# Kernel optimization log

Measured on AMD Instinct MI355X. Metric: run time of the kernel, lower is better.

Reference implementation:

```python
import jax, jax.numpy as jnp
import numpy as np

# ---- static config (matches init_kwargs) ----
C, H, W = 3, 224, 224
P = 16
KH, KW = H // P, W // P          # 14, 14
N_PATCH = KH * KW                # 196
PATCH_ELEMS = C * P * P          # 768
D = 768
HEADS = 12
Y = 64                            # head dim
M = 3072                          # hopfield memories
N_MASK = 100
NSTEPS = 12
ALPHA = 0.1
BETA = 1.0 / float(np.sqrt(Y))
EPS = 1e-5
B = 16


def lnorm(x, gamma, delta):
    # EnergyLayerNorm: scalar gamma, vector delta, RMS of centered x
    xm = x - x.mean(-1, keepdims=True)
    return gamma * xm / jnp.sqrt((xm * xm).mean(-1, keepdims=True) + EPS) + delta


def energy(g, Wq, Wk, Xi):
    # attention energy: -(1/beta) sum_h sum_q logsumexp_k(beta * q_h . k_h)
    q = jnp.einsum('nd,hdy->nhy', g, Wq)
    k = jnp.einsum('nd,hdy->nhy', g, Wk)
    A = jnp.einsum('nhy,mhy->hnm', q, k)                    # [H, N, N]
    e_att = -(1.0 / BETA) * jax.nn.logsumexp(BETA * A, axis=-1).sum()
    # hopfield energy: -0.5 * sum relu(g @ Xi)^2
    hid = jax.nn.relu(g @ Xi)                                # [N, M]
    e_hn = -0.5 * jnp.sum(hid * hid)
    return e_att + e_hn


def patchify(img):
    # (C, H, W) -> (n_patches, C*P*P), matching '... c (kh h) (kw w) -> ... (kh kw) c h w' then flatten c h w
    x = img.reshape(C, KH, P, KW, P).transpose(1, 3, 0, 2, 4)
    return x.reshape(N_PATCH, PATCH_ELEMS)


def unpatchify(p):
    # (n_patches, C, P, P) -> (C, H, W)
    return p.reshape(KH, KW, C, P, P).transpose(2, 0, 3, 1, 4).reshape(C, H, W)


def forward_single(img, mask, enc_W, enc_b, dec_W, dec_b, cls_token, mask_token,
                   pos_embed, Wq, Wk, Xi, gamma, delta):
    tok = patchify(img) @ enc_W + enc_b                      # [N_PATCH, D]
    (idx,) = jnp.nonzero(mask == 1, size=N_MASK, fill_value=0)
    tok = tok.at[idx].set(mask_token)                        # corrupt masked tokens
    x = jnp.concatenate([cls_token[None], tok], axis=0) + pos_embed  # [N_PATCH+1, D]
    grad_e = jax.grad(energy)
    for _ in range(NSTEPS):
        g = lnorm(x, gamma, delta)
        x = x - ALPHA * grad_e(g, Wq, Wk, Xi)
    x = x[1:]
    g = lnorm(x, gamma, delta)
    dec = (g @ dec_W + dec_b).reshape(N_PATCH, C, P, P)
    return unpatchify(dec)


def setup_inputs() -> dict:
    key = jax.random.key(0)
    ks = jax.random.split(key, 10)
    return {
        'x': jax.random.normal(ks[0], (B, C, H, W), dtype=jnp.float32),
        'mask': jax.random.randint(ks[1], (B, N_PATCH), 0, 2, dtype=jnp.int32),
        'enc_W': 0.1 * jax.random.normal(ks[2], (PATCH_ELEMS, D), dtype=jnp.float32),
        'enc_b': jnp.zeros((D,), dtype=jnp.float32),
        'dec_W': 0.1 * jax.random.normal(ks[3], (D, PATCH_ELEMS), dtype=jnp.float32),
        'dec_b': jnp.zeros((PATCH_ELEMS,), dtype=jnp.float32),
        'cls_token': 0.002 * jax.random.normal(ks[4], (D,), dtype=jnp.float32),
        'mask_token': 0.002 * jax.random.normal(ks[5], (D,), dtype=jnp.float32),
        'pos_embed': 0.002 * jax.random.normal(ks[6], (1 + N_PATCH, D), dtype=jnp.float32),
        'Wq': 0.02 * jax.random.normal(ks[7], (HEADS, D, Y), dtype=jnp.float32),
        'Wk': 0.02 * jax.random.normal(ks[8], (HEADS, D, Y), dtype=jnp.float32),
        'Xi': 0.02 * jax.random.normal(ks[9], (D, M), dtype=jnp.float32),
        'gamma': jnp.ones((), dtype=jnp.float32),
        'delta': jnp.zeros((D,), dtype=jnp.float32),
    }


def reference(x, mask, enc_W, enc_b, dec_W, dec_b, cls_token, mask_token,
              pos_embed, Wq, Wk, Xi, gamma, delta):
    f = jax.vmap(forward_single, in_axes=(0, 0) + (None,) * 12)
    return f(x, mask, enc_W, enc_b, dec_W, dec_b, cls_token, mask_token,
             pos_embed, Wq, Wk, Xi, gamma, delta)
```

## Files before the change

kernel.cpp:

```cpp
#include <hip/hip_runtime.h>
#include <math.h>

#define C_      3
#define H_      224
#define W_      224
#define KH_     14
#define KW_     14
#define NPATCH  196
#define PELEMS  768
#define D_      768
#define HEADS_  12
#define Y_      64
#define MHID    3072
#define NMASK   100
#define NSTEPS  12
#define ALPHA_  0.1f
#define BETA_   0.125f
#define EPS_    1e-5f
#define B_      16
#define NTOK    197
#define ROWS    (B_*NTOK)
#define MPAD    3200
#define QKLD    1536
#define PACKLD  4608
#define W2LD    4608
#define KSPLIT  4

typedef short short8 __attribute__((ext_vector_type(8)));
typedef unsigned short ushort8 __attribute__((ext_vector_type(8)));
typedef float floatx4 __attribute__((ext_vector_type(4)));

__device__ __forceinline__ unsigned short f2bf(float f) {
    union { float f; unsigned u; } v; v.f = f;
    unsigned r = (v.u + 0x7FFFu + ((v.u >> 16) & 1u)) >> 16;
    return (unsigned short)r;
}
__device__ __forceinline__ float bf2f(unsigned short u) {
    union { unsigned u; float f; } v; v.u = ((unsigned)u) << 16;
    return v.f;
}

__device__ __forceinline__ void async_cp16(const void* g, void* l) {
    __builtin_amdgcn_global_load_lds(
        (const __attribute__((address_space(1))) unsigned int*)g,
        (__attribute__((address_space(3))) unsigned int*)l, 16, 0, 0);
}

template<int OUT_MODE, bool RELU, bool HAS_BIAS>
__global__ __launch_bounds__(256) void mfma_gemm(
    const unsigned short* __restrict__ A, int lda,
    const unsigned short* __restrict__ B, int ldb,
    void* __restrict__ Cout, int ldc, void* __restrict__ Cout2,
    const float* __restrict__ bias, int K)
{
    __shared__ alignas(16) unsigned short ldsA[2][64 * 32];
    __shared__ alignas(16) unsigned short ldsB[2][128 * 32];

    const int bx = blockIdx.x, by = blockIdx.y;
    const int koff = (OUT_MODE == 4) ? blockIdx.z * K : 0;

    const int t    = threadIdx.x;
    const int wave = t >> 6;
    const int lane = t & 63;
    const int row0 = by << 6;
    const int col0 = bx << 7;
    const int wm = (wave & 1) << 5;
    const int wn = (wave >> 1) << 6;
    const int r  = lane & 15;
    const int qd = lane >> 4;

    const unsigned short* Abase = A + (size_t)row0 * lda + koff;
    const unsigned short* Bbase = B + (size_t)col0 * ldb + koff;

    floatx4 acc[2][4];
#pragma unroll
    for (int i = 0; i < 2; ++i)
#pragma unroll
        for (int j = 0; j < 4; ++j)
            acc[i][j] = (floatx4){0.f, 0.f, 0.f, 0.f};

    const int crow = t >> 2;
    const int coff = (t & 3) << 3;
    for (int k0 = 0; k0 < K; k0 += 64) {
#pragma unroll
        for (int kb = 0; kb < 2; ++kb) {
            const int kk = k0 + kb * 32;
            async_cp16(Abase + (size_t)crow * lda + kk + coff,
                       ldsA[kb] + (wave << 9));
            async_cp16(Bbase + (size_t)crow * ldb + kk + coff,
                       ldsB[kb] + (wave << 9));
            async_cp16(Bbase + (size_t)(64 + crow) * ldb + kk + coff,
                       ldsB[kb] + 2048 + (wave << 9));
        }
        __syncthreads();
#pragma unroll
        for (int kb = 0; kb < 2; ++kb) {
            short8 af[2], bfr[4];
#pragma unroll
            for (int i = 0; i < 2; ++i)
                af[i]  = *(const short8*)&ldsA[kb][(wm + (i << 4) + r) * 32 + (qd << 3)];
#pragma unroll
            for (int j = 0; j < 4; ++j)
                bfr[j] = *(const short8*)&ldsB[kb][(wn + (j << 4) + r) * 32 + (qd << 3)];
#pragma unroll
            for (int i = 0; i < 2; ++i)
#pragma unroll
                for (int j = 0; j < 4; ++j)
                    acc[i][j] = __builtin_amdgcn_mfma_f32_16x16x32_bf16(
                                    af[i], bfr[j], acc[i][j], 0, 0, 0);
        }
        __syncthreads();
    }

#pragma unroll
    for (int i = 0; i < 2; ++i) {
#pragma unroll
        for (int j = 0; j < 4; ++j) {
            int cc = col0 + wn + (j << 4) + r;
#pragma unroll
            for (int reg = 0; reg < 4; ++reg) {
                int rr = row0 + wm + (i << 4) + (qd << 2) + reg;
                float v = acc[i][j][reg];
                if (HAS_BIAS) v += bias[cc];
                if (RELU)     v = fmaxf(v, 0.f);
                if (OUT_MODE == 1)
                    ((unsigned short*)Cout)[(size_t)rr * ldc + cc] = f2bf(v);
                else if (OUT_MODE == 3) {
                    if (cc < QKLD)
                        ((unsigned short*)Cout)[(size_t)rr * QKLD + cc] = f2bf(v);
                    else
                        ((unsigned short*)Cout2)[(size_t)rr * PACKLD + (cc - QKLD)]
                            = f2bf(fmaxf(v, 0.f));
                } else if (OUT_MODE == 4)
                    atomicAdd(&((float*)Cout)[(size_t)rr * ldc + cc], ALPHA_ * v);
                else
                    ((float*)Cout)[(size_t)rr * ldc + cc] = v;
            }
        }
    }
}

__global__ __launch_bounds__(512) void attn_fused_kernel(
    const unsigned short* __restrict__ qk,
    unsigned short* __restrict__ pack)
{
    __shared__ alignas(16) unsigned short Ks[208 * 72];
    __shared__ alignas(16) unsigned short Kt[64 * 232];
    __shared__ alignas(16) unsigned short Qc[32 * 72];
    __shared__ alignas(16) unsigned short Qtc[64 * 40];
    __shared__ alignas(16) unsigned short Pb[32 * 232];
    __shared__ alignas(16) unsigned short PTb[208 * 40];
    __shared__ alignas(16) float Pm[32 * 212];

    const int bh = blockIdx.x;
    const int h = bh % HEADS_, b = bh / HEADS_;
    const int t = threadIdx.x;
    const int lane = t & 63, wave = t >> 6;
    const int ln15 = lane & 15, quad = lane >> 4;
    const size_t rowbase = (size_t)(b * NTOK) * QKLD;
    const int hoff = h * 64;

    for (int idx = t; idx < 208 * 8; idx += 512) {
        int m = idx >> 3, c8 = idx & 7;
        uint4 v = (uint4){0, 0, 0, 0};
        if (m < NTOK)
            v = *(const uint4*)&qk[rowbase + (size_t)m * QKLD + 768 + hoff + c8 * 8];
        *(uint4*)&Ks[m * 72 + c8 * 8] = v;
    }
    for (int idx = t; idx < (32 * 232) / 8; idx += 512)
        *(uint4*)&Pb[idx * 8] = (uint4){0, 0, 0, 0};
    for (int idx = t; idx < (208 * 40) / 8; idx += 512)
        *(uint4*)&PTb[idx * 8] = (uint4){0, 0, 0, 0};
    __syncthreads();

    for (int idx = t; idx < 64 * 112; idx += 512) {
        int y = idx / 112, mp = idx % 112;
        int m0 = 2 * mp;
        unsigned lo = (m0     < 208) ? Ks[(m0    ) * 72 + y] : 0u;
        unsigned hi = (m0 + 1 < 208) ? Ks[(m0 + 1) * 72 + y] : 0u;
        *(unsigned*)&Kt[y * 232 + m0] = lo | (hi << 16);
    }
    __syncthreads();

    floatx4 gk[7];
#pragma unroll
    for (int i = 0; i < 7; ++i) gk[i] = (floatx4){0.f, 0.f, 0.f, 0.f};

    for (int nc = 0; nc < 7; ++nc) {
        const int n0 = nc * 32;
        const int csz = (NTOK - n0 < 32) ? (NTOK - n0) : 32;

        for (int idx = t; idx < 32 * 8; idx += 512) {
            int nn = idx >> 3, c8 = idx & 7;
            uint4 v = (uint4){0, 0, 0, 0};
            if (nn < csz)
                v = *(const uint4*)&qk[rowbase + (size_t)(n0 + nn) * QKLD + hoff + c8 * 8];
            *(uint4*)&Qc[nn * 72 + c8 * 8] = v;
        }
        __syncthreads();

        for (int idx = t; idx < 64 * 16; idx += 512) {
            int y = idx >> 4, np = idx & 15;
            unsigned lo = Qc[(2 * np    ) * 72 + y];
            unsigned hi = Qc[(2 * np + 1) * 72 + y];
            *(unsigned*)&Qtc[y * 40 + 2 * np] = lo | (hi << 16);
        }

        {
            short8 aq[2][2];
#pragma unroll
            for (int nt = 0; nt < 2; ++nt)
#pragma unroll
                for (int kb = 0; kb < 2; ++kb)
                    aq[nt][kb] = *(const short8*)
                        &Qc[(nt * 16 + ln15) * 72 + kb * 32 + quad * 8];

            for (int mt = wave; mt < 13; mt += 8) {
                short8 b0 = *(const short8*)&Ks[(mt * 16 + ln15) * 72 + quad * 8];
                short8 b1 = *(const short8*)&Ks[(mt * 16 + ln15) * 72 + 32 + quad * 8];
                floatx4 s0 = (floatx4){0.f, 0.f, 0.f, 0.f};
                floatx4 s1 = (floatx4){0.f, 0.f, 0.f, 0.f};
                s0 = __builtin_amdgcn_mfma_f32_16x16x32_bf16(aq[0][0], b0, s0, 0, 0, 0);
                s0 = __builtin_amdgcn_mfma_f32_16x16x32_bf16(aq[0][1], b1, s0, 0, 0, 0);
                s1 = __builtin_amdgcn_mfma_f32_16x16x32_bf16(aq[1][0], b0, s1, 0, 0, 0);
                s1 = __builtin_amdgcn_mfma_f32_16x16x32_bf16(aq[1][1], b1, s1, 0, 0, 0);
#pragma unroll
                for (int reg = 0; reg < 4; ++reg) {
                    Pm[(quad * 4 + reg) * 212 + mt * 16 + ln15]      = s0[reg];
                    Pm[(16 + quad * 4 + reg) * 212 + mt * 16 + ln15] = s1[reg];
                }
            }
        }
        __syncthreads();

        for (int nn = wave; nn < csz; nn += 8) {
            float v0 = Pm[nn * 212 + lane];
            float v1 = (lane +  64 < NTOK) ? Pm[nn * 212 + lane +  64] : -1e30f;
            float v2 = (lane + 128 < NTOK) ? Pm[nn * 212 + lane + 128] : -1e30f;
            float v3 = (lane + 192 < NTOK) ? Pm[nn * 212 + lane + 192] : -1e30f;
            float mx = fmaxf(fmaxf(v0, v1), fmaxf(v2, v3));
#pragma unroll
            for (int o = 32; o > 0; o >>= 1) mx = fmaxf(mx, __shfl_xor(mx, o, 64));
            float e0 = __expf((v0 - mx) * BETA_);
            float e1 = (lane +  64 < NTOK) ? __expf((v1 - mx) * BETA_) : 0.f;
            float e2 = (lane + 128 < NTOK) ? __expf((v2 - mx) * BETA_) : 0.f;
            float e3 = (lane + 192 < NTOK) ? __expf((v3 - mx) * BETA_) : 0.f;
            float s = e0 + e1 + e2 + e3;
#pragma unroll
            for (int o = 32; o > 0; o >>= 1) s += __shfl_xor(s, o, 64);
            float inv = 1.0f / s;
            {
                unsigned short p = f2bf(e0 * inv);
                Pb[nn * 232 + lane] = p;
                PTb[lane * 40 + nn] = p;
            }
            {
                unsigned short p = f2bf(e1 * inv);
                Pb[nn * 232 + lane + 64] = p;
                PTb[(lane + 64) * 40 + nn] = p;
            }
            {
                unsigned short p = f2bf(e2 * inv);
                Pb[nn * 232 + lane + 128] = p;
                PTb[(lane + 128) * 40 + nn] = p;
            }
            if (lane + 192 < NTOK) {
                unsigned short p = f2bf(e3 * inv);
                Pb[nn * 232 + lane + 192] = p;
                PTb[(lane + 192) * 40 + nn] = p;
            }
        }
        __syncthreads();

        {
            const int nt = wave >> 2, yt = wave & 3;
            floatx4 gq = (floatx4){0.f, 0.f, 0.f, 0.f};
#pragma unroll
            for (int ks = 0; ks < 7; ++ks) {
                short8 a  = *(const short8*)&Pb[(nt * 16 + ln15) * 232 + ks * 32 + quad * 8];
                short8 bk = *(const short8*)&Kt[(yt * 16 + ln15) * 232 + ks * 32 + quad * 8];
                gq = __builtin_amdgcn_mfma_f32_16x16x32_bf16(a, bk, gq, 0, 0, 0);
            }
#pragma unroll
            for (int reg = 0; reg < 4; ++reg) {
                int row = nt * 16 + quad * 4 + reg;
                if (row < csz)
                    pack[(size_t)(b * NTOK + n0 + row) * PACKLD
                         + 3072 + hoff + yt * 16 + ln15] = f2bf(gq[reg]);
            }
        }

#pragma unroll
        for (int i = 0; i < 7; ++i) {
            int ti = wave + i * 8;
            if (ti < 52) {
                int mt = ti >> 2, yt = ti & 3;
                short8 a  = *(const short8*)&PTb[(mt * 16 + ln15) * 40 + quad * 8];
                short8 bq = *(const short8*)&Qtc[(yt * 16 + ln15) * 40 + quad * 8];
                gk[i] = __builtin_amdgcn_mfma_f32_16x16x32_bf16(a, bq, gk[i], 0, 0, 0);
            }
        }
    }

#pragma unroll
    for (int i = 0; i < 7; ++i) {
        int ti = wave + i * 8;
        if (ti < 52) {
            int mt = ti >> 2, yt = ti & 3;
#pragma unroll
            for (int reg = 0; reg < 4; ++reg) {
                int m = mt * 16 + quad * 4 + reg;
                if (m < NTOK)
                    pack[(size_t)(b * NTOK + m) * PACKLD
                         + 3840 + hoff + yt * 16 + ln15] = f2bf(gk[i][reg]);
            }
        }
    }
}

__global__ __launch_bounds__(256) void w2pack_kernel(const float* __restrict__ Wq,
                                                     const float* __restrict__ Wk,
                                                     const float* __restrict__ Xi,
                                                     unsigned short* __restrict__ out)
{
    int idx = blockIdx.x * 256 + threadIdx.x;
    int d = idx % D_, n = idx / D_;
    float v;
    if (n < 768)       v = Wq[((size_t)(n >> 6) * D_ + d) * Y_ + (n & 63)];
    else if (n < 1536) { int e = n - 768; v = Wk[((size_t)(e >> 6) * D_ + d) * Y_ + (e & 63)]; }
    else               v = Xi[(size_t)d * MHID + (n - 1536)];
    out[idx] = f2bf(v);
}

__global__ __launch_bounds__(256) void bpack_kernel(const float* __restrict__ Xi,
                                                    const float* __restrict__ Wq,
                                                    const float* __restrict__ Wk,
                                                    unsigned short* __restrict__ out)
{
    int idx = blockIdx.x * 256 + threadIdx.x;
    int c = idx % PACKLD, d = idx / PACKLD;
    float v;
    if (c < 3072)       v = Xi[(size_t)d * MHID + c];
    else if (c < 3840)  { int e = c - 3072; v = Wq[((size_t)(e >> 6) * D_ + d) * Y_ + (e & 63)]; }
    else                { int e = c - 3840; v = Wk[((size_t)(e >> 6) * D_ + d) * Y_ + (e & 63)]; }
    out[idx] = f2bf(v);
}

__global__ __launch_bounds__(256) void t768_kernel(const float* __restrict__ in,
                                                   unsigned short* __restrict__ out)
{
    int idx = blockIdx.x * 256 + threadIdx.x;
    int k = idx % D_, n = idx / D_;
    out[idx] = f2bf(in[(size_t)k * D_ + n]);
}

__global__ void mask_flags_kernel(const int* __restrict__ mask, int* __restrict__ flags)
{
    int b = threadIdx.x;
    if (b >= B_) return;
    const int* mb = mask + b * NPATCH;
    int* fb = flags + b * NPATCH;
    int cnt = 0;
    for (int n = 0; n < NPATCH; ++n) {
        int mv = mb[n];
        fb[n] = (mv == 1 && cnt < NMASK) ? 1 : 0;
        cnt += (mv == 1);
    }
    if (cnt < NMASK) fb[0] = 1;
}

__global__ __launch_bounds__(256) void patchify_kernel(const float* __restrict__ img,
                                                       unsigned short* __restrict__ patch)
{
    int idx = blockIdx.x * 256 + threadIdx.x;
    int e = idx % PELEMS, row = idx / PELEMS;
    int b = row / NPATCH, n = row % NPATCH;
    int kh = n / KW_, kw = n % KW_;
    int c = e >> 8, p = (e >> 4) & 15, q2 = e & 15;
    patch[idx] = f2bf(img[(((size_t)b * C_ + c) * H_ + kh * 16 + p) * W_ + kw * 16 + q2]);
}

__global__ __launch_bounds__(256) void build_x_kernel(const float* __restrict__ tok,
                                                      const int* __restrict__ flags,
                                                      const float* __restrict__ cls,
                                                      const float* __restrict__ mtok,
                                                      const float* __restrict__ pos,
                                                      float* __restrict__ x)
{
    int row = blockIdx.x;
    int b = row / NTOK, rr = row % NTOK;
    int tid = threadIdx.x;
#pragma unroll
    for (int i = 0; i < 3; ++i) {
        int d = tid + (i << 8);
        float v;
        if (rr == 0) v = cls[d];
        else {
            int n = rr - 1;
            v = flags[b * NPATCH + n] ? mtok[d]
                                      : tok[((size_t)b * NPATCH + n) * D_ + d];
        }
        x[(size_t)row * D_ + d] = v + pos[(size_t)rr * D_ + d];
    }
}

__global__ __launch_bounds__(256) void lnorm_kernel(const float* __restrict__ x,
                                                    unsigned short* __restrict__ g,
                                                    const float* __restrict__ gamma,
                                                    const float* __restrict__ delta)
{
    int row = blockIdx.x, tid = threadIdx.x;
    const float* xr = x + (size_t)row * D_;
    float v0 = xr[tid], v1 = xr[tid + 256], v2 = xr[tid + 512];

    __shared__ float red[256];
    red[tid] = v0 + v1 + v2;
    __syncthreads();
    for (int off = 128; off > 0; off >>= 1) {
        if (tid < off) red[tid] += red[tid + off];
        __syncthreads();
    }
    float mean = red[0] * (1.0f / D_);
    __syncthreads();
    float a0 = v0 - mean, a1 = v1 - mean, a2 = v2 - mean;
    red[tid] = a0 * a0 + a1 * a1 + a2 * a2;
    __syncthreads();
    for (int off = 128; off > 0; off >>= 1) {
        if (tid < off) red[tid] += red[tid + off];
        __syncthreads();
    }
    float var = red[0] * (1.0f / D_);
    float inv = gamma[0] / sqrtf(var + EPS_);
    unsigned short* gr = g + (size_t)row * D_;
    gr[tid]       = f2bf(a0 * inv + delta[tid]);
    gr[tid + 256] = f2bf(a1 * inv + delta[tid + 256]);
    gr[tid + 512] = f2bf(a2 * inv + delta[tid + 512]);
}

__global__ __launch_bounds__(256) void unpatch_kernel(const float* __restrict__ dec,
                                                      float* __restrict__ out)
{
    int idx = blockIdx.x * 256 + threadIdx.x;
    int ww = idx % W_;
    int t2 = idx / W_;
    int hh = t2 % H_;
    int t3 = t2 / H_;
    int c  = t3 % C_;
    int b  = t3 / C_;
    int kh = hh >> 4, p = hh & 15, kw = ww >> 4, q2 = ww & 15;
    int n = kh * KW_ + kw;
    int e = (c << 8) + (p << 4) + q2;
    out[idx] = dec[((size_t)b * NTOK + 1 + n) * D_ + e];
}

extern "C" void kernel_launch(void* const* d_in, const int* in_sizes, int n_in,
                              void* d_out, int out_size, void* d_ws, size_t ws_size,
                              hipStream_t stream)
{
    const float* img   = (const float*)d_in[0];
    const int*   mask  = (const int*)d_in[1];
    const float* enc_W = (const float*)d_in[2];
    const float* enc_b = (const float*)d_in[3];
    const float* dec_W = (const float*)d_in[4];
    const float* dec_b = (const float*)d_in[5];
    const float* cls   = (const float*)d_in[6];
    const float* mtok  = (const float*)d_in[7];
    const float* pos   = (const float*)d_in[8];
    const float* Wq    = (const float*)d_in[9];
    const float* Wk    = (const float*)d_in[10];
    const float* Xi    = (const float*)d_in[11];
    const float* gamma = (const float*)d_in[12];
    const float* delta = (const float*)d_in[13];
    float* out = (float*)d_out;

    float* ws = (float*)d_ws;
    size_t off = 0;
    auto alloc = [&](size_t nfloats) {
        off = (off + 63) & ~(size_t)63;
        float* p = ws + off; off += nfloats; return p;
    };
    float*          x    = alloc((size_t)MPAD * D_);
    unsigned short* g    = (unsigned short*)alloc((size_t)MPAD * D_ / 2);
    unsigned short* qkg  = (unsigned short*)alloc((size_t)MPAD * QKLD / 2);
    float*          decb = (float*)qkg;
    unsigned short* pack = (unsigned short*)alloc((size_t)MPAD * PACKLD / 2);
    unsigned short* W2   = (unsigned short*)alloc((size_t)W2LD * D_ / 2);
    unsigned short* Bpk  = (unsigned short*)alloc((size_t)D_ * PACKLD / 2);
    unsigned short* decT = (unsigned short*)alloc((size_t)D_ * D_ / 2);
    unsigned short* encT = (unsigned short*)alloc((size_t)D_ * D_ / 2);
    int*            flags = (int*)alloc(B_ * NPATCH);
    unsigned short* patch = pack;
    float*          tok   = (float*)(pack + (size_t)MPAD * D_);

    const dim3 blk(256);

    w2pack_kernel<<<dim3(W2LD * D_ / 256), blk, 0, stream>>>(Wq, Wk, Xi, W2);
    bpack_kernel<<<dim3(D_ * PACKLD / 256), blk, 0, stream>>>(Xi, Wq, Wk, Bpk);
    t768_kernel<<<dim3(D_ * D_ / 256), blk, 0, stream>>>(dec_W, decT);
    t768_kernel<<<dim3(D_ * D_ / 256), blk, 0, stream>>>(enc_W, encT);
    mask_flags_kernel<<<dim3(1), dim3(64), 0, stream>>>(mask, flags);

    patchify_kernel<<<dim3(B_ * NPATCH * PELEMS / 256), blk, 0, stream>>>(img, patch);
    mfma_gemm<0, false, true><<<dim3(D_ / 128, MPAD / 64), blk, 0, stream>>>(
        patch, PELEMS, encT, PELEMS, tok, D_, nullptr, enc_b, PELEMS);
    build_x_kernel<<<dim3(ROWS), blk, 0, stream>>>(tok, flags, cls, mtok, pos, x);

    for (int step = 0; step < NSTEPS; ++step) {
        lnorm_kernel<<<dim3(ROWS), blk, 0, stream>>>(x, g, gamma, delta);
        mfma_gemm<3, false, false><<<dim3(W2LD / 128, MPAD / 64), blk, 0, stream>>>(
            g, D_, W2, D_, qkg, QKLD, pack, nullptr, D_);
        attn_fused_kernel<<<dim3(B_ * HEADS_), dim3(512), 0, stream>>>(qkg, pack);
        mfma_gemm<4, false, false><<<dim3(D_ / 128, MPAD / 64, KSPLIT), blk, 0, stream>>>(
            pack, PACKLD, Bpk, PACKLD, x, D_, nullptr, nullptr, PACKLD / KSPLIT);
    }

    lnorm_kernel<<<dim3(ROWS), blk, 0, stream>>>(x, g, gamma, delta);
    mfma_gemm<0, false, true><<<dim3(D_ / 128, MPAD / 64), blk, 0, stream>>>(
        g, D_, decT, D_, decb, D_, nullptr, dec_b, D_);
    unpatch_kernel<<<dim3(B_ * C_ * H_ * W_ / 256), blk, 0, stream>>>(decb, out);
}
```

Before: 1.831 ms.

## Double-buffer LDS tiles in MFMA GEMM to overlap global loads with compute

Adds a second LDS buffer for the A and B tiles in the bf16 MFMA GEMM. The first tile is prefetched before the loop, and each iteration issues async loads for the next K-slab before computing on the current one, with a single barrier per iteration. This hides global-to-LDS load latency behind MFMA work, at the cost of doubled shared memory per block and possibly lower occupancy.

Result: slower. 1.912 ms (+4.4%).

```diff
diff --git a/kernel.cpp b/kernel.cpp
--- a/kernel.cpp
+++ b/kernel.cpp
@@ -53,8 +53,8 @@
     void* __restrict__ Cout, int ldc, void* __restrict__ Cout2,
     const float* __restrict__ bias, int K)
 {
-    __shared__ alignas(16) unsigned short ldsA[2][64 * 32];
-    __shared__ alignas(16) unsigned short ldsB[2][128 * 32];
+    __shared__ alignas(16) unsigned short ldsA[2][2][64 * 32];
+    __shared__ alignas(16) unsigned short ldsB[2][2][128 * 32];
 
     const int bx = blockIdx.x, by = blockIdx.y;
     const int koff = (OUT_MODE == 4) ? blockIdx.z * K : 0;
@@ -81,27 +81,43 @@
 
     const int crow = t >> 2;
     const int coff = (t & 3) << 3;
+
+#pragma unroll
+    for (int kb = 0; kb < 2; ++kb) {
+        const int kk = kb * 32;
+        async_cp16(Abase + (size_t)crow * lda + kk + coff,
+                   ldsA[0][kb] + (wave << 9));
+        async_cp16(Bbase + (size_t)crow * ldb + kk + coff,
+                   ldsB[0][kb] + (wave << 9));
+        async_cp16(Bbase + (size_t)(64 + crow) * ldb + kk + coff,
+                   ldsB[0][kb] + 2048 + (wave << 9));
+    }
+    __syncthreads();
+
+    int cur = 0;
     for (int k0 = 0; k0 < K; k0 += 64) {
-#pragma unroll
-        for (int kb = 0; kb < 2; ++kb) {
-            const int kk = k0 + kb * 32;
-            async_cp16(Abase + (size_t)crow * lda + kk + coff,
-                       ldsA[kb] + (wave << 9));
-            async_cp16(Bbase + (size_t)crow * ldb + kk + coff,
-                       ldsB[kb] + (wave << 9));
-            async_cp16(Bbase + (size_t)(64 + crow) * ldb + kk + coff,
-                       ldsB[kb] + 2048 + (wave << 9));
-        }
-        __syncthreads();
+        if (k0 + 64 < K) {
+            const int nxt = cur ^ 1;
+#pragma unroll
+            for (int kb = 0; kb < 2; ++kb) {
+                const int kk = k0 + 64 + kb * 32;
+                async_cp16(Abase + (size_t)crow * lda + kk + coff,
+                           ldsA[nxt][kb] + (wave << 9));
+                async_cp16(Bbase + (size_t)crow * ldb + kk + coff,
+                           ldsB[nxt][kb] + (wave << 9));
+                async_cp16(Bbase + (size_t)(64 + crow) * ldb + kk + coff,
+                           ldsB[nxt][kb] + 2048 + (wave << 9));
+            }
+        }
 #pragma unroll
         for (int kb = 0; kb < 2; ++kb) {
             short8 af[2], bfr[4];
 #pragma unroll
             for (int i = 0; i < 2; ++i)
-                af[i]  = *(const short8*)&ldsA[kb][(wm + (i << 4) + r) * 32 + (qd << 3)];
+                af[i]  = *(const short8*)&ldsA[cur][kb][(wm + (i << 4) + r) * 32 + (qd << 3)];
 #pragma unroll
             for (int j = 0; j < 4; ++j)
-                bfr[j] = *(const short8*)&ldsB[kb][(wn + (j << 4) + r) * 32 + (qd << 3)];
+                bfr[j] = *(const short8*)&ldsB[cur][kb][(wn + (j << 4) + r) * 32 + (qd << 3)];
 #pragma unroll
             for (int i = 0; i < 2; ++i)
 #pragma unroll
@@ -110,6 +126,7 @@
                                     af[i], bfr[j], acc[i][j], 0, 0, 0);
         }
         __syncthreads();
+        cur ^= 1;
     }
 
 #pragma unroll
```
